# Kernel tuning notes

Hardware: AMD Instinct MI355X
Metric: run time of the kernel (lower is better)

## Reference

```python
import jax, jax.numpy as jnp
import numpy as np

N_HEAD, D_MODEL, D_K, D_V, MAX_NEIGHBOR = 8, 512, 64, 64, 5
BS, SEQ = 2, 1024


def setup_inputs() -> dict:
    key = jax.random.key(0)
    ks = jax.random.split(key, 12)
    inp = {
        'q': jax.random.normal(ks[0], (BS, SEQ, D_MODEL), jnp.float32),
        'k': jax.random.normal(ks[1], (BS, SEQ, D_MODEL), jnp.float32),
        'v': jax.random.normal(ks[2], (BS, SEQ, D_MODEL), jnp.float32),
        'mask': jnp.ones((BS, SEQ, SEQ), jnp.int32),
        'dist': jax.random.randint(ks[3], (BS, SEQ, SEQ), 0, 10, jnp.int32),
        # weights stored as (in, out) so y = x @ W
        'w_qs': jax.random.normal(ks[4], (D_MODEL, N_HEAD * D_K), jnp.float32) * 0.02,
        'w_ks': jax.random.normal(ks[5], (D_MODEL, N_HEAD * D_K), jnp.float32) * 0.02,
        'w_vs': jax.random.normal(ks[6], (D_MODEL, N_HEAD * D_V), jnp.float32) * 0.02,
        'w_fc': jax.random.normal(ks[7], (N_HEAD * D_V, D_MODEL), jnp.float32) * 0.02,
        'ln_gamma': jnp.ones((D_MODEL,), jnp.float32),
        'ln_beta': jnp.zeros((D_MODEL,), jnp.float32),
        'base_rpr': jax.random.normal(ks[8], (MAX_NEIGHBOR + 1, D_K), jnp.float32) * 0.02,
    }
    return inp


def reference(q, k, v, mask, dist, w_qs, w_ks, w_vs, w_fc, ln_gamma, ln_beta, base_rpr):
    bs, sq, dm = q.shape
    temp = jnp.asarray(D_K, q.dtype) ** 0.5
    residual = q
    # layer norm on q only (as in original)
    mu = jnp.mean(q, axis=-1, keepdims=True)
    var = jnp.var(q, axis=-1, keepdims=True)
    qn = (q - mu) / jnp.sqrt(var + 1e-6) * ln_gamma + ln_beta
    # projections -> [bs, heads, seq, d]
    qh = (qn @ w_qs).reshape(bs, sq, N_HEAD, D_K).transpose(0, 2, 1, 3)
    kh = (k @ w_ks).reshape(bs, sq, N_HEAD, D_K).transpose(0, 2, 1, 3)
    vh = (v @ w_vs).reshape(bs, sq, N_HEAD, D_V).transpose(0, 2, 1, 3)
    qs = qh / temp
    # standard QK^T scores
    attn1 = jnp.einsum('bhid,bhjd->bhij', qs, kh)
    # relative-position scores: instead of materializing rpr[b,i,j,d],
    # contract q with the small base table then gather by clipped distance.
    dc = jnp.minimum(dist, MAX_NEIGHBOR)  # dist>max_neighbor -> max_neighbor
    qb = jnp.einsum('bhid,md->bhim', qs, base_rpr)  # [bs,h,seq,M+1]
    idx = jnp.broadcast_to(dc[:, None, :, :], (bs, N_HEAD, sq, sq))
    attn2 = jnp.take_along_axis(qb, idx, axis=-1)  # [bs,h,seq,seq]
    attn = attn1 + attn2
    attn = jnp.where(mask[:, None, :, :] == 0, jnp.asarray(-1e9, attn.dtype), attn)
    attn = jax.nn.softmax(attn, axis=-1)  # dropout disabled (eval)
    out = jnp.einsum('bhij,bhjd->bhid', attn, vh)
    out = out.transpose(0, 2, 1, 3).reshape(bs, sq, N_HEAD * D_V)
    out = out @ w_fc + residual
    return out, attn
```

## Files before the change

### kernel.cpp

```cpp
#include <hip/hip_runtime.h>
#include <math.h>

#define SEQ 1024
#define DM 512

typedef __attribute__((ext_vector_type(8))) short bf16x8;
typedef __attribute__((ext_vector_type(4))) short bf16x4;
typedef __attribute__((ext_vector_type(4))) float f32x4;
typedef __attribute__((ext_vector_type(4))) int i32x4;

static __device__ __forceinline__ short f2b(float f) {
    union { float f; unsigned u; } x; x.f = f;
    unsigned r = (x.u + 0x7FFFu + ((x.u >> 16) & 1u)) >> 16;
    return (short)r;
}
static __device__ __forceinline__ float b2f(short s) {
    union { unsigned u; float f; } x; x.u = ((unsigned)(unsigned short)s) << 16;
    return x.f;
}
static __device__ __forceinline__ int sidx(int row, int col) {
    int byte = (row << 7) + (col << 1);
    byte ^= (row & 7) << 4;
    return byte >> 1;
}

static __device__ __forceinline__ void stage_f32(short* dst, const float* src, int srcStride, int tid) {
    int r = tid >> 2, c = (tid & 3) * 16;
    const float* p = src + (size_t)r * srcStride + c;
    bf16x8 v0, v1;
    #pragma unroll
    for (int e = 0; e < 8; ++e) v0[e] = f2b(p[e]);
    #pragma unroll
    for (int e = 0; e < 8; ++e) v1[e] = f2b(p[8 + e]);
    *(bf16x8*)&dst[sidx(r, c)] = v0;
    *(bf16x8*)&dst[sidx(r, c + 8)] = v1;
}
static __device__ __forceinline__ void stage_bf16(short* dst, const short* src, int srcStride, int tid) {
    int r = tid >> 2, c = (tid & 3) * 16;
    const short* p = src + (size_t)r * srcStride + c;
    bf16x8 v0 = *(const bf16x8*)p;
    bf16x8 v1 = *(const bf16x8*)(p + 8);
    *(bf16x8*)&dst[sidx(r, c)] = v0;
    *(bf16x8*)&dst[sidx(r, c + 8)] = v1;
}

static __device__ __forceinline__ void mma64(const short* sA, const short* sB, f32x4* acc,
                                             int w, int lr, int lg) {
    #pragma unroll
    for (int ks = 0; ks < 2; ++ks) {
        bf16x8 af = *(const bf16x8*)&sA[sidx(w * 16 + lr, ks * 32 + lg * 8)];
        #pragma unroll
        for (int nt = 0; nt < 4; ++nt) {
            bf16x8 bf = *(const bf16x8*)&sB[sidx(nt * 16 + lr, ks * 32 + lg * 8)];
            acc[nt] = __builtin_amdgcn_mfma_f32_16x16x32_bf16(af, bf, acc[nt], 0, 0, 0);
        }
    }
}

__global__ __launch_bounds__(256) void prep_kernel(
    const float* __restrict__ w0, const float* __restrict__ w1,
    const float* __restrict__ w2, const float* __restrict__ w3, short* __restrict__ wt,
    const float* __restrict__ q, float* __restrict__ qn,
    const float* __restrict__ gamma, const float* __restrict__ beta,
    const int* __restrict__ dist, const int* __restrict__ mask, unsigned char* __restrict__ idxp) {
    int blk = blockIdx.x;
    int tid = threadIdx.x;
    if (blk < 256) {
        int wsel = blk >> 6;
        int t = blk & 63;
        int tr = t >> 3, tc = t & 7;
        const float* src = wsel == 0 ? w0 : wsel == 1 ? w1 : wsel == 2 ? w2 : w3;
        short* dst = wt + (size_t)wsel * 512 * 512;
        __shared__ float tile[64][65];
        int r = tid >> 2, c = (tid & 3) * 16;
        const float* p = src + (size_t)(tr * 64 + r) * 512 + tc * 64 + c;
        #pragma unroll
        for (int e = 0; e < 16; ++e) tile[r][c + e] = p[e];
        __syncthreads();
        bf16x8 v0, v1;
        #pragma unroll
        for (int e = 0; e < 16; ++e) {
            short bv = f2b(tile[c + e][r]);
            if (e < 8) v0[e] = bv; else v1[e - 8] = bv;
        }
        short* qd = dst + (size_t)(tc * 64 + r) * 512 + tr * 64 + c;
        *(bf16x8*)qd = v0;
        *(bf16x8*)(qd + 8) = v1;
    } else if (blk < 2304) {
        int row = blk - 256;
        const float* x = q + (size_t)row * DM;
        float* y = qn + (size_t)row * DM;
        float v1 = x[tid], v2 = x[tid + 256];
        float s = v1 + v2;
        float ss = v1 * v1 + v2 * v2;
        for (int o = 32; o > 0; o >>= 1) { s += __shfl_down(s, o); ss += __shfl_down(ss, o); }
        __shared__ float red[4], red2[4];
        __shared__ float s_mu, s_rstd;
        int wid = tid >> 6, lane = tid & 63;
        if (lane == 0) { red[wid] = s; red2[wid] = ss; }
        __syncthreads();
        if (tid == 0) {
            float ts = red[0] + red[1] + red[2] + red[3];
            float tss = red2[0] + red2[1] + red2[2] + red2[3];
            float mu = ts / DM;
            float var = tss / DM - mu * mu;
            s_mu = mu;
            s_rstd = rsqrtf(var + 1e-6f);
        }
        __syncthreads();
        float mu = s_mu, rstd = s_rstd;
        y[tid]       = (v1 - mu) * rstd * gamma[tid]       + beta[tid];
        y[tid + 256] = (v2 - mu) * rstd * gamma[tid + 256] + beta[tid + 256];
    } else {
        size_t base = ((size_t)(blk - 2304) * 256 + tid) * 8;
        i32x4 d0 = *(const i32x4*)(dist + base);
        i32x4 d1 = *(const i32x4*)(dist + base + 4);
        i32x4 m0 = *(const i32x4*)(mask + base);
        i32x4 m1 = *(const i32x4*)(mask + base + 4);
        int dv[8], mv[8];
        #pragma unroll
        for (int e = 0; e < 4; ++e) { dv[e] = d0[e]; dv[4 + e] = d1[e]; mv[e] = m0[e]; mv[4 + e] = m1[e]; }
        unsigned char ob[4];
        #pragma unroll
        for (int e = 0; e < 4; ++e) {
            int dA = dv[2 * e];     if (dA > 5) dA = 5;
            int dB = dv[2 * e + 1]; if (dB > 5) dB = 5;
            unsigned nA = (unsigned)dA | (mv[2 * e] == 0 ? 8u : 0u);
            unsigned nB = (unsigned)dB | (mv[2 * e + 1] == 0 ? 8u : 0u);
            ob[e] = (unsigned char)(nA | (nB << 4));
        }
        *(uchar4*)(idxp + base / 2) = *(uchar4*)ob;
    }
}

__global__ __launch_bounds__(256) void qkv_kernel(
    const float* __restrict__ qn, const float* __restrict__ k, const float* __restrict__ v,
    const short* __restrict__ wT, short* __restrict__ qsb, short* __restrict__ khx,
    short* __restrict__ vfx) {
    __shared__ short sA[64 * 64];
    __shared__ short sB[64 * 64];
    int tid = threadIdx.x;
    int sel = blockIdx.x >> 8;
    int t = blockIdx.x & 255;
    int bx = t & 7, by = t >> 3;
    int m0 = by << 6, n0 = bx << 6;
    int w = tid >> 6, l = tid & 63;
    int lr = l & 15, lg = l >> 4;
    const float* A = sel == 0 ? qn : sel == 1 ? k : v;
    const short* Bt = wT + (size_t)sel * 262144;
    float scale = sel == 0 ? 0.125f : 1.0f;
    f32x4 acc[4] = {};
    for (int kt = 0; kt < 512; kt += 64) {
        __syncthreads();
        stage_f32(sA, A + (size_t)m0 * 512 + kt, 512, tid);
        stage_bf16(sB, Bt + (size_t)n0 * 512 + kt, 512, tid);
        __syncthreads();
        mma64(sA, sB, acc, w, lr, lg);
    }
    short* scratch = sA + w * 1024;
    if (sel == 0) {
        #pragma unroll
        for (int nt = 0; nt < 4; ++nt)
            #pragma unroll
            for (int r = 0; r < 4; ++r)
                scratch[(lg * 4 + r) * 64 + nt * 16 + lr] = f2b(acc[nt][r] * scale);
        #pragma unroll
        for (int cc = 0; cc < 2; ++cc) {
            int c = cc * 64 + l;
            *(bf16x8*)&qsb[(size_t)(m0 + w * 16 + (c >> 3)) * 512 + n0 + (c & 7) * 8]
                = *(const bf16x8*)&scratch[c * 8];
        }
    } else if (sel == 1) {
        #pragma unroll
        for (int nt = 0; nt < 4; ++nt) {
            int dl = nt * 16 + lr;
            int f = dl >> 5, lgp = (dl >> 3) & 3, e = dl & 7;
            int base = ((f * 4 + lgp) * 16) * 8 + e;
            #pragma unroll
            for (int r = 0; r < 4; ++r)
                scratch[base + (lg * 4 + r) * 8] = f2b(acc[nt][r]);
        }
        int bq = m0 >> 10, jt = (m0 >> 6) & 15;
        short* blockp = khx + ((((size_t)(bq * 8 + bx) * 16 + jt) * 4 + w) << 10);
        *(bf16x8*)(blockp + l * 8)       = *(const bf16x8*)(scratch + l * 8);
        *(bf16x8*)(blockp + 512 + l * 8) = *(const bf16x8*)(scratch + 512 + l * 8);
    } else {
        int bq = m0 >> 10, j6 = (m0 >> 6) & 15, p = j6 >> 1, rel = j6 & 1;
        #pragma unroll
        for (int nt = 0; nt < 4; ++nt)
            #pragma unroll
            for (int r = 0; r < 4; ++r) {
                int s = ((nt * 2 + (lg >> 1)) * 16 + lr) * 8 + (lg & 1) * 4 + r;
                scratch[s] = f2b(acc[nt][r]);
            }
        short* blockp = vfx + ((((size_t)(bq * 8 + bx) * 8 + p) * 4 + w) << 11);
        #pragma unroll
        for (int cc = 0; cc < 2; ++cc) {
            int c = cc * 64 + l;
            int s = c * 8;
            int g = s + ((c >> 5) << 8) + (rel << 8);
            *(bf16x8*)(blockp + g) = *(const bf16x8*)(scratch + s);
        }
    }
}

#define IDXSTR 520
__global__ __launch_bounds__(256) void attn_fused_kernel(
    const short* __restrict__ qsb, const short* __restrict__ khx,
    const short* __restrict__ vfx, const unsigned char* __restrict__ idxp,
    const float* __restrict__ rpr, float* __restrict__ attnp, short* __restrict__ oh) {
    int bid = blockIdx.x;
    int bh = bid >> 6, it = bid & 63;
    int b = bh >> 3, h = bh & 7;
    int i0 = it << 4;
    int tid = threadIdx.x;
    int w = tid >> 6, l = tid & 63;
    int lr = l & 15, lg = l >> 4;

    __shared__ short sQ[16 * 64];
    __shared__ float sQB[16 * 8];
    __shared__ float sL[4][16];
    __shared__ float sO[4 * 16 * 64];
    __shared__ __align__(16) unsigned char sIdx[16 * IDXSTR];

    if (tid < 128) {
        int r = tid >> 3, c = (tid & 7) * 8;
        bf16x8 qv = *(const bf16x8*)(qsb + ((size_t)(b * SEQ + i0 + r)) * DM + h * 64 + c);
        *(bf16x8*)&sQ[sidx(r, c)] = qv;
    }
    {
        const unsigned char* ibase = idxp + ((size_t)(b * SEQ + i0)) * 512;
        #pragma unroll
        for (int p = 0; p < 2; ++p) {
            int idx = p * 256 + tid;
            int row = idx >> 5;
            int cb = (idx & 31) * 16;
            i32x4 v = *(const i32x4*)(ibase + (size_t)row * 512 + cb);
            *(i32x4*)&sIdx[row * IDXSTR + cb] = v;
        }
    }
    __syncthreads();
    if (tid < 128) {
        int r = tid >> 3, m = tid & 7;
        if (m < 6) {
            float a = 0.f;
            #pragma unroll 8
            for (int d = 0; d < 64; ++d) a += b2f(sQ[sidx(r, d)]) * rpr[m * 64 + d];
            sQB[r * 8 + m] = a;
        }
    }
    __syncthreads();

    bf16x8 qf0 = *(const bf16x8*)&sQ[sidx(lr, lg * 8)];
    bf16x8 qf1 = *(const bf16x8*)&sQ[sidx(lr, 32 + lg * 8)];

    float qb0 = sQB[lr * 8 + 0], qb1 = sQB[lr * 8 + 1], qb2 = sQB[lr * 8 + 2];
    float qb3 = sQB[lr * 8 + 3], qb4 = sQB[lr * 8 + 4], qb5 = sQB[lr * 8 + 5];

    float l_lane = 0.f;
    unsigned p_lo[16], p_hi[16];
    f32x4 accO[4] = {};
    const short* kblk = khx + (((size_t)bh * 16) * 4 + w) * 1024;
    const short* vblk = vfx + (((size_t)bh * 8) * 4 + w) * 2048;
    int fragoff = (lg * 16 + lr) * 8;
    const unsigned char* irow = sIdx + lr * IDXSTR + w * 8 + lg * 2;

    #pragma unroll
    for (int jt = 0; jt < 16; ++jt) {
        const short* kb = kblk + jt * 4096;
        bf16x8 kf0 = *(const bf16x8*)(kb + fragoff);
        bf16x8 kf1 = *(const bf16x8*)(kb + 512 + fragoff);
        f32x4 sf = {};
        sf = __builtin_amdgcn_mfma_f32_16x16x32_bf16(kf0, qf0, sf, 0, 0, 0);
        sf = __builtin_amdgcn_mfma_f32_16x16x32_bf16(kf1, qf1, sf, 0, 0, 0);
        unsigned u = *(const unsigned short*)(irow + jt * 32);
        float pv[4];
        #pragma unroll
        for (int r = 0; r < 4; ++r) {
            unsigned bb = (u >> (4 * r)) & 0xFu;
            unsigned dd = bb & 7u;
            float t0 = (dd & 1) ? qb1 : qb0;
            float t1 = (dd & 1) ? qb3 : qb2;
            float t2 = (dd & 1) ? qb5 : qb4;
            float u0 = (dd & 2) ? t1 : t0;
            float bias = (dd & 4) ? t2 : u0;
            float s = fminf(sf[r] + bias, 30.f);
            float p = (bb & 8) ? 0.f : __expf(s);
            pv[r] = p;
            l_lane += p;
        }
        unsigned plo, phi;
        asm("v_cvt_pk_bf16_f32 %0, %1, %2" : "=v"(plo) : "v"(pv[0]), "v"(pv[1]));
        asm("v_cvt_pk_bf16_f32 %0, %1, %2" : "=v"(phi) : "v"(pv[2]), "v"(pv[3]));
        p_lo[jt] = plo; p_hi[jt] = phi;
        if (jt & 1) {
            unsigned plo0 = p_lo[jt - 1], phi0 = p_hi[jt - 1];
            int srcA = lr + ((lg & 1) << 5);
            int srcB = srcA + 16;
            unsigned aw0 = __shfl(plo0, srcA), aw1 = __shfl(phi0, srcA);
            unsigned aw2 = __shfl(plo,  srcA), aw3 = __shfl(phi,  srcA);
            unsigned bw0 = __shfl(plo0, srcB), bw1 = __shfl(phi0, srcB);
            unsigned bw2 = __shfl(plo,  srcB), bw3 = __shfl(phi,  srcB);
            bool hi = lg >= 2;
            union { unsigned q[4]; bf16x8 v; } afu;
            afu.q[0] = hi ? aw2 : aw0;
            afu.q[1] = hi ? aw3 : aw1;
            afu.q[2] = hi ? bw2 : bw0;
            afu.q[3] = hi ? bw3 : bw1;
            bf16x8 af = afu.v;
            const short* vb = vblk + (jt >> 1) * 8192;
            #pragma unroll
            for (int nt = 0; nt < 4; ++nt) {
                bf16x8 bf = *(const bf16x8*)(vb + nt * 512 + fragoff);
                accO[nt] = __builtin_amdgcn_mfma_f32_16x16x32_bf16(af, bf, accO[nt], 0, 0, 0);
            }
        }
    }

    l_lane += __shfl_xor(l_lane, 16);
    l_lane += __shfl_xor(l_lane, 32);
    if (lg == 0) sL[w][lr] = l_lane;
    #pragma unroll
    for (int nt = 0; nt < 4; ++nt)
        #pragma unroll
        for (int r = 0; r < 4; ++r)
            sO[w * 1024 + (lg * 4 + r) * 64 + nt * 16 + lr] = accO[nt][r];
    __syncthreads();

    {
        int row = tid >> 4, c4 = (tid & 15) * 4;
        f32x4 o = *(f32x4*)&sO[row * 64 + c4];
        o += *(f32x4*)&sO[1024 + row * 64 + c4];
        o += *(f32x4*)&sO[2048 + row * 64 + c4];
        o += *(f32x4*)&sO[3072 + row * 64 + c4];
        float rl = 1.f / (sL[0][row] + sL[1][row] + sL[2][row] + sL[3][row]);
        bf16x4 ob;
        #pragma unroll
        for (int e = 0; e < 4; ++e) ob[e] = f2b(o[e] * rl);
        *(bf16x4*)&oh[((size_t)(b * SEQ + i0 + row)) * DM + h * 64 + c4] = ob;
    }

    float rl = 1.f / (sL[0][lr] + sL[1][lr] + sL[2][lr] + sL[3][lr]);
    float* ap = attnp + ((size_t)(bh * SEQ + i0 + lr)) * SEQ + w * 16 + lg * 4;
    #pragma unroll
    for (int jt = 0; jt < 16; ++jt) {
        unsigned plo = p_lo[jt], phi = p_hi[jt];
        f32x4 o;
        o[0] = b2f((short)(plo & 0xffff)) * rl;
        o[1] = b2f((short)(plo >> 16))    * rl;
        o[2] = b2f((short)(phi & 0xffff)) * rl;
        o[3] = b2f((short)(phi >> 16))    * rl;
        *(f32x4*)&ap[jt * 64] = o;
    }
}

__global__ __launch_bounds__(256) void fc_kernel(
    const short* __restrict__ oh, const short* __restrict__ BtFc,
    const float* __restrict__ Rsd, float* __restrict__ Cp) {
    __shared__ short sA[64 * 64];
    __shared__ short sB[64 * 64];
    int tid = threadIdx.x;
    int bx = blockIdx.x & 7, by = blockIdx.x >> 3;
    int m0 = by << 6, n0 = bx << 6;
    int w = tid >> 6, l = tid & 63;
    int lr = l & 15, lg = l >> 4;
    f32x4 acc[4] = {};
    for (int kt = 0; kt < 512; kt += 64) {
        __syncthreads();
        stage_bf16(sA, oh + (size_t)m0 * 512 + kt, 512, tid);
        stage_bf16(sB, BtFc + (size_t)n0 * 512 + kt, 512, tid);
        __syncthreads();
        mma64(sA, sB, acc, w, lr, lg);
    }
    #pragma unroll
    for (int nt = 0; nt < 4; ++nt)
        #pragma unroll
        for (int r = 0; r < 4; ++r) {
            int gm = m0 + w * 16 + lg * 4 + r;
            int gn = n0 + nt * 16 + lr;
            Cp[(size_t)gm * 512 + gn] = acc[nt][r] + Rsd[(size_t)gm * 512 + gn];
        }
}

extern "C" void kernel_launch(void* const* d_in, const int* in_sizes, int n_in,
                              void* d_out, int out_size, void* d_ws, size_t ws_size,
                              hipStream_t stream) {
    const float* q     = (const float*)d_in[0];
    const float* k     = (const float*)d_in[1];
    const float* v     = (const float*)d_in[2];
    const int*   mask  = (const int*)d_in[3];
    const int*   dist  = (const int*)d_in[4];
    const float* w_qs  = (const float*)d_in[5];
    const float* w_ks  = (const float*)d_in[6];
    const float* w_vs  = (const float*)d_in[7];
    const float* w_fc  = (const float*)d_in[8];
    const float* gamma = (const float*)d_in[9];
    const float* beta  = (const float*)d_in[10];
    const float* rpr   = (const float*)d_in[11];

    char* wsb = (char*)d_ws;
    float* qn   = (float*)wsb;
    short* oh   = (short*)wsb;
    short* wT   = (short*)(wsb + 4u * 1024 * 1024);
    short* qsb  = (short*)(wsb + 6u * 1024 * 1024);
    short* khx  = (short*)(wsb + 8u * 1024 * 1024);
    short* vfx  = (short*)(wsb + 10u * 1024 * 1024);
    unsigned char* idxp = (unsigned char*)(wsb + 12u * 1024 * 1024);

    float* outp  = (float*)d_out;
    float* attnp = outp + 1048576;

    prep_kernel<<<3328, 256, 0, stream>>>(w_qs, w_ks, w_vs, w_fc, wT, q, qn, gamma, beta, dist, mask, idxp);
    qkv_kernel<<<768, 256, 0, stream>>>(qn, k, v, wT, qsb, khx, vfx);
    attn_fused_kernel<<<1024, 256, 0, stream>>>(qsb, khx, vfx, idxp, rpr, attnp, oh);
    fc_kernel<<<256, 256, 0, stream>>>(oh, wT + 786432, q, outp);
}
```

Measured before the change: 70.48 us.

## Process 32 query rows per attention block to reuse K/V fragments

Each attention block now handles two 16-row query tiles, so every K and V fragment loaded from global memory feeds two sets of MFMAs, and half as many blocks are launched. Shared memory is aliased: the output-reduction buffer overlays the Q, bias and index buffers to keep LDS use down. The cost is roughly double the register pressure (two probability arrays and two accumulator sets), which may reduce occupancy or cause spills, and only 512 blocks remain to fill the GPU.

```diff
diff --git a/kernel.cpp b/kernel.cpp
--- a/kernel.cpp
+++ b/kernel.cpp
@@ -210,20 +210,21 @@
     const short* __restrict__ vfx, const unsigned char* __restrict__ idxp,
     const float* __restrict__ rpr, float* __restrict__ attnp, short* __restrict__ oh) {
     int bid = blockIdx.x;
-    int bh = bid >> 6, it = bid & 63;
+    int bh = bid >> 5, it = bid & 31;
     int b = bh >> 3, h = bh & 7;
-    int i0 = it << 4;
+    int i0 = it << 5;
     int tid = threadIdx.x;
     int w = tid >> 6, l = tid & 63;
     int lr = l & 15, lg = l >> 4;
 
-    __shared__ short sQ[16 * 64];
-    __shared__ float sQB[16 * 8];
-    __shared__ float sL[4][16];
-    __shared__ float sO[4 * 16 * 64];
-    __shared__ __align__(16) unsigned char sIdx[16 * IDXSTR];
-
-    if (tid < 128) {
+    __shared__ __align__(16) char sBuf[21764];
+    __shared__ float sL[4][32];
+    short* sQ = (short*)sBuf;
+    float* sQB = (float*)(sBuf + 4096);
+    unsigned char* sIdx = (unsigned char*)(sBuf + 5120);
+    float* sO = (float*)sBuf;
+
+    {
         int r = tid >> 3, c = (tid & 7) * 8;
         bf16x8 qv = *(const bf16x8*)(qsb + ((size_t)(b * SEQ + i0 + r)) * DM + h * 64 + c);
         *(bf16x8*)&sQ[sidx(r, c)] = qv;
@@ -231,7 +232,7 @@
     {
         const unsigned char* ibase = idxp + ((size_t)(b * SEQ + i0)) * 512;
         #pragma unroll
-        for (int p = 0; p < 2; ++p) {
+        for (int p = 0; p < 4; ++p) {
             int idx = p * 256 + tid;
             int row = idx >> 5;
             int cb = (idx & 31) * 16;
@@ -240,7 +241,7 @@
         }
     }
     __syncthreads();
-    if (tid < 128) {
+    {
         int r = tid >> 3, m = tid & 7;
         if (m < 6) {
             float a = 0.f;
@@ -251,82 +252,125 @@
     }
     __syncthreads();
 
-    bf16x8 qf0 = *(const bf16x8*)&sQ[sidx(lr, lg * 8)];
-    bf16x8 qf1 = *(const bf16x8*)&sQ[sidx(lr, 32 + lg * 8)];
-
-    float qb0 = sQB[lr * 8 + 0], qb1 = sQB[lr * 8 + 1], qb2 = sQB[lr * 8 + 2];
-    float qb3 = sQB[lr * 8 + 3], qb4 = sQB[lr * 8 + 4], qb5 = sQB[lr * 8 + 5];
-
-    float l_lane = 0.f;
-    unsigned p_lo[16], p_hi[16];
-    f32x4 accO[4] = {};
+    bf16x8 qfA0 = *(const bf16x8*)&sQ[sidx(lr, lg * 8)];
+    bf16x8 qfA1 = *(const bf16x8*)&sQ[sidx(lr, 32 + lg * 8)];
+    bf16x8 qfB0 = *(const bf16x8*)&sQ[sidx(16 + lr, lg * 8)];
+    bf16x8 qfB1 = *(const bf16x8*)&sQ[sidx(16 + lr, 32 + lg * 8)];
+
+    float qa0 = sQB[lr * 8 + 0], qa1 = sQB[lr * 8 + 1], qa2 = sQB[lr * 8 + 2];
+    float qa3 = sQB[lr * 8 + 3], qa4 = sQB[lr * 8 + 4], qa5 = sQB[lr * 8 + 5];
+    float qc0 = sQB[(16 + lr) * 8 + 0], qc1 = sQB[(16 + lr) * 8 + 1], qc2 = sQB[(16 + lr) * 8 + 2];
+    float qc3 = sQB[(16 + lr) * 8 + 3], qc4 = sQB[(16 + lr) * 8 + 4], qc5 = sQB[(16 + lr) * 8 + 5];
+
+    float lA = 0.f, lB = 0.f;
+    unsigned pAlo[16], pAhi[16], pBlo[16], pBhi[16];
+    f32x4 accA[4] = {}, accB[4] = {};
     const short* kblk = khx + (((size_t)bh * 16) * 4 + w) * 1024;
     const short* vblk = vfx + (((size_t)bh * 8) * 4 + w) * 2048;
     int fragoff = (lg * 16 + lr) * 8;
-    const unsigned char* irow = sIdx + lr * IDXSTR + w * 8 + lg * 2;
+    const unsigned char* irowA = sIdx + lr * IDXSTR + w * 8 + lg * 2;
+    const unsigned char* irowB = sIdx + (16 + lr) * IDXSTR + w * 8 + lg * 2;
 
     #pragma unroll
     for (int jt = 0; jt < 16; ++jt) {
         const short* kb = kblk + jt * 4096;
         bf16x8 kf0 = *(const bf16x8*)(kb + fragoff);
         bf16x8 kf1 = *(const bf16x8*)(kb + 512 + fragoff);
-        f32x4 sf = {};
-        sf = __builtin_amdgcn_mfma_f32_16x16x32_bf16(kf0, qf0, sf, 0, 0, 0);
-        sf = __builtin_amdgcn_mfma_f32_16x16x32_bf16(kf1, qf1, sf, 0, 0, 0);
-        unsigned u = *(const unsigned short*)(irow + jt * 32);
-        float pv[4];
+        f32x4 sfA = {}, sfB = {};
+        sfA = __builtin_amdgcn_mfma_f32_16x16x32_bf16(kf0, qfA0, sfA, 0, 0, 0);
+        sfA = __builtin_amdgcn_mfma_f32_16x16x32_bf16(kf1, qfA1, sfA, 0, 0, 0);
+        sfB = __builtin_amdgcn_mfma_f32_16x16x32_bf16(kf0, qfB0, sfB, 0, 0, 0);
+        sfB = __builtin_amdgcn_mfma_f32_16x16x32_bf16(kf1, qfB1, sfB, 0, 0, 0);
+        unsigned uA = *(const unsigned short*)(irowA + jt * 32);
+        unsigned uB = *(const unsigned short*)(irowB + jt * 32);
+        float pvA[4], pvB[4];
         #pragma unroll
         for (int r = 0; r < 4; ++r) {
-            unsigned bb = (u >> (4 * r)) & 0xFu;
+            unsigned bb = (uA >> (4 * r)) & 0xFu;
             unsigned dd = bb & 7u;
-            float t0 = (dd & 1) ? qb1 : qb0;
-            float t1 = (dd & 1) ? qb3 : qb2;
-            float t2 = (dd & 1) ? qb5 : qb4;
+            float t0 = (dd & 1) ? qa1 : qa0;
+            float t1 = (dd & 1) ? qa3 : qa2;
+            float t2 = (dd & 1) ? qa5 : qa4;
             float u0 = (dd & 2) ? t1 : t0;
             float bias = (dd & 4) ? t2 : u0;
-            float s = fminf(sf[r] + bias, 30.f);
+            float s = fminf(sfA[r] + bias, 30.f);
             float p = (bb & 8) ? 0.f : __expf(s);
-            pv[r] = p;
-            l_lane += p;
-        }
-        unsigned plo, phi;
-        asm("v_cvt_pk_bf16_f32 %0, %1, %2" : "=v"(plo) : "v"(pv[0]), "v"(pv[1]));
-        asm("v_cvt_pk_bf16_f32 %0, %1, %2" : "=v"(phi) : "v"(pv[2]), "v"(pv[3]));
-        p_lo[jt] = plo; p_hi[jt] = phi;
+            pvA[r] = p; lA += p;
+        }
+        #pragma unroll
+        for (int r = 0; r < 4; ++r) {
+            unsigned bb = (uB >> (4 * r)) & 0xFu;
+            unsigned dd = bb & 7u;
+            float t0 = (dd & 1) ? qc1 : qc0;
+            float t1 = (dd & 1) ? qc3 : qc2;
+            float t2 = (dd & 1) ? qc5 : qc4;
+            float u0 = (dd & 2) ? t1 : t0;
+            float bias = (dd & 4) ? t2 : u0;
+            float s = fminf(sfB[r] + bias, 30.f);
+            float p = (bb & 8) ? 0.f : __expf(s);
+            pvB[r] = p; lB += p;
+        }
+        unsigned a0, a1, b0, b1;
+        asm("v_cvt_pk_bf16_f32 %0, %1, %2" : "=v"(a0) : "v"(pvA[0]), "v"(pvA[1]));
+        asm("v_cvt_pk_bf16_f32 %0, %1, %2" : "=v"(a1) : "v"(pvA[2]), "v"(pvA[3]));
+        asm("v_cvt_pk_bf16_f32 %0, %1, %2" : "=v"(b0) : "v"(pvB[0]), "v"(pvB[1]));
+        asm("v_cvt_pk_bf16_f32 %0, %1, %2" : "=v"(b1) : "v"(pvB[2]), "v"(pvB[3]));
+        pAlo[jt] = a0; pAhi[jt] = a1; pBlo[jt] = b0; pBhi[jt] = b1;
         if (jt & 1) {
-            unsigned plo0 = p_lo[jt - 1], phi0 = p_hi[jt - 1];
             int srcA = lr + ((lg & 1) << 5);
             int srcB = srcA + 16;
-            unsigned aw0 = __shfl(plo0, srcA), aw1 = __shfl(phi0, srcA);
-            unsigned aw2 = __shfl(plo,  srcA), aw3 = __shfl(phi,  srcA);
-            unsigned bw0 = __shfl(plo0, srcB), bw1 = __shfl(phi0, srcB);
-            unsigned bw2 = __shfl(plo,  srcB), bw3 = __shfl(phi,  srcB);
+            const short* vb = vblk + (jt >> 1) * 8192;
+            bf16x8 vf0 = *(const bf16x8*)(vb + 0 * 512 + fragoff);
+            bf16x8 vf1 = *(const bf16x8*)(vb + 1 * 512 + fragoff);
+            bf16x8 vf2 = *(const bf16x8*)(vb + 2 * 512 + fragoff);
+            bf16x8 vf3 = *(const bf16x8*)(vb + 3 * 512 + fragoff);
             bool hi = lg >= 2;
-            union { unsigned q[4]; bf16x8 v; } afu;
-            afu.q[0] = hi ? aw2 : aw0;
-            afu.q[1] = hi ? aw3 : aw1;
-            afu.q[2] = hi ? bw2 : bw0;
-            afu.q[3] = hi ? bw3 : bw1;
-            bf16x8 af = afu.v;
-            const short* vb = vblk + (jt >> 1) * 8192;
-            #pragma unroll
-            for (int nt = 0; nt < 4; ++nt) {
-                bf16x8 bf = *(const bf16x8*)(vb + nt * 512 + fragoff);
-                accO[nt] = __builtin_amdgcn_mfma_f32_16x16x32_bf16(af, bf, accO[nt], 0, 0, 0);
+            {
+                unsigned plo0 = pAlo[jt - 1], phi0 = pAhi[jt - 1];
+                unsigned aw0 = __shfl(plo0, srcA), aw1 = __shfl(phi0, srcA);
+                unsigned aw2 = __shfl(a0,  srcA), aw3 = __shfl(a1,  srcA);
+                unsigned bw0 = __shfl(plo0, srcB), bw1 = __shfl(phi0, srcB);
+                unsigned bw2 = __shfl(a0,  srcB), bw3 = __shfl(a1,  srcB);
+                union { unsigned q[4]; bf16x8 v; } afu;
+                afu.q[0] = hi ? aw2 : aw0;
+                afu.q[1] = hi ? aw3 : aw1;
+                afu.q[2] = hi ? bw2 : bw0;
+                afu.q[3] = hi ? bw3 : bw1;
+                accA[0] = __builtin_amdgcn_mfma_f32_16x16x32_bf16(afu.v, vf0, accA[0], 0, 0, 0);
+                accA[1] = __builtin_amdgcn_mfma_f32_16x16x32_bf16(afu.v, vf1, accA[1], 0, 0, 0);
+                accA[2] = __builtin_amdgcn_mfma_f32_16x16x32_bf16(afu.v, vf2, accA[2], 0, 0, 0);
+                accA[3] = __builtin_amdgcn_mfma_f32_16x16x32_bf16(afu.v, vf3, accA[3], 0, 0, 0);
             }
-        }
-    }
-
-    l_lane += __shfl_xor(l_lane, 16);
-    l_lane += __shfl_xor(l_lane, 32);
-    if (lg == 0) sL[w][lr] = l_lane;
+            {
+                unsigned plo0 = pBlo[jt - 1], phi0 = pBhi[jt - 1];
+                unsigned aw0 = __shfl(plo0, srcA), aw1 = __shfl(phi0, srcA);
+                unsigned aw2 = __shfl(b0,  srcA), aw3 = __shfl(b1,  srcA);
+                unsigned bw0 = __shfl(plo0, srcB), bw1 = __shfl(phi0, srcB);
+                unsigned bw2 = __shfl(b0,  srcB), bw3 = __shfl(b1,  srcB);
+                union { unsigned q[4]; bf16x8 v; } afu;
+                afu.q[0] = hi ? aw2 : aw0;
+                afu.q[1] = hi ? aw3 : aw1;
+                afu.q[2] = hi ? bw2 : bw0;
+                afu.q[3] = hi ? bw3 : bw1;
+                accB[0] = __builtin_amdgcn_mfma_f32_16x16x32_bf16(afu.v, vf0, accB[0], 0, 0, 0);
+                accB[1] = __builtin_amdgcn_mfma_f32_16x16x32_bf16(afu.v, vf1, accB[1], 0, 0, 0);
+                accB[2] = __builtin_amdgcn_mfma_f32_16x16x32_bf16(afu.v, vf2, accB[2], 0, 0, 0);
+                accB[3] = __builtin_amdgcn_mfma_f32_16x16x32_bf16(afu.v, vf3, accB[3], 0, 0, 0);
+            }
+        }
+    }
+
+    lA += __shfl_xor(lA, 16); lA += __shfl_xor(lA, 32);
+    lB += __shfl_xor(lB, 16); lB += __shfl_xor(lB, 32);
+    if (lg == 0) { sL[w][lr] = lA; sL[w][16 + lr] = lB; }
+    __syncthreads();
+
     #pragma unroll
     for (int nt = 0; nt < 4; ++nt)
         #pragma unroll
         for (int r = 0; r < 4; ++r)
-            sO[w * 1024 + (lg * 4 + r) * 64 + nt * 16 + lr] = accO[nt][r];
-    __syncthreads();
-
+            sO[w * 1024 + (lg * 4 + r) * 64 + nt * 16 + lr] = accA[nt][r];
+    __syncthreads();
     {
         int row = tid >> 4, c4 = (tid & 15) * 4;
         f32x4 o = *(f32x4*)&sO[row * 64 + c4];
@@ -339,18 +383,44 @@
         for (int e = 0; e < 4; ++e) ob[e] = f2b(o[e] * rl);
         *(bf16x4*)&oh[((size_t)(b * SEQ + i0 + row)) * DM + h * 64 + c4] = ob;
     }
-
-    float rl = 1.f / (sL[0][lr] + sL[1][lr] + sL[2][lr] + sL[3][lr]);
-    float* ap = attnp + ((size_t)(bh * SEQ + i0 + lr)) * SEQ + w * 16 + lg * 4;
+    __syncthreads();
+    #pragma unroll
+    for (int nt = 0; nt < 4; ++nt)
+        #pragma unroll
+        for (int r = 0; r < 4; ++r)
+            sO[w * 1024 + (lg * 4 + r) * 64 + nt * 16 + lr] = accB[nt][r];
+    __syncthreads();
+    {
+        int row = tid >> 4, c4 = (tid & 15) * 4;
+        f32x4 o = *(f32x4*)&sO[row * 64 + c4];
+        o += *(f32x4*)&sO[1024 + row * 64 + c4];
+        o += *(f32x4*)&sO[2048 + row * 64 + c4];
+        o += *(f32x4*)&sO[3072 + row * 64 + c4];
+        float rl = 1.f / (sL[0][16 + row] + sL[1][16 + row] + sL[2][16 + row] + sL[3][16 + row]);
+        bf16x4 ob;
+        #pragma unroll
+        for (int e = 0; e < 4; ++e) ob[e] = f2b(o[e] * rl);
+        *(bf16x4*)&oh[((size_t)(b * SEQ + i0 + 16 + row)) * DM + h * 64 + c4] = ob;
+    }
+
+    float rlA = 1.f / (sL[0][lr] + sL[1][lr] + sL[2][lr] + sL[3][lr]);
+    float rlB = 1.f / (sL[0][16 + lr] + sL[1][16 + lr] + sL[2][16 + lr] + sL[3][16 + lr]);
+    float* apA = attnp + ((size_t)(bh * SEQ + i0 + lr)) * SEQ + w * 16 + lg * 4;
+    float* apB = attnp + ((size_t)(bh * SEQ + i0 + 16 + lr)) * SEQ + w * 16 + lg * 4;
     #pragma unroll
     for (int jt = 0; jt < 16; ++jt) {
-        unsigned plo = p_lo[jt], phi = p_hi[jt];
         f32x4 o;
-        o[0] = b2f((short)(plo & 0xffff)) * rl;
-        o[1] = b2f((short)(plo >> 16))    * rl;
-        o[2] = b2f((short)(phi & 0xffff)) * rl;
-        o[3] = b2f((short)(phi >> 16))    * rl;
-        *(f32x4*)&ap[jt * 64] = o;
+        o[0] = b2f((short)(pAlo[jt] & 0xffff)) * rlA;
+        o[1] = b2f((short)(pAlo[jt] >> 16))    * rlA;
+        o[2] = b2f((short)(pAhi[jt] & 0xffff)) * rlA;
+        o[3] = b2f((short)(pAhi[jt] >> 16))    * rlA;
+        *(f32x4*)&apA[jt * 64] = o;
+        f32x4 o2;
+        o2[0] = b2f((short)(pBlo[jt] & 0xffff)) * rlB;
+        o2[1] = b2f((short)(pBlo[jt] >> 16))    * rlB;
+        o2[2] = b2f((short)(pBhi[jt] & 0xffff)) * rlB;
+        o2[3] = b2f((short)(pBhi[jt] >> 16))    * rlB;
+        *(f32x4*)&apB[jt * 64] = o2;
     }
 }
 
@@ -412,6 +482,6 @@
 
     prep_kernel<<<3328, 256, 0, stream>>>(w_qs, w_ks, w_vs, w_fc, wT, q, qn, gamma, beta, dist, mask, idxp);
     qkv_kernel<<<768, 256, 0, stream>>>(qn, k, v, wT, qsb, khx, vfx);
-    attn_fused_kernel<<<1024, 256, 0, stream>>>(qsb, khx, vfx, idxp, rpr, attnp, oh);
+    attn_fused_kernel<<<512, 256, 0, stream>>>(qsb, khx, vfx, idxp, rpr, attnp, oh);
     fc_kernel<<<256, 256, 0, stream>>>(oh, wT + 786432, q, outp);
 }
```

New measurement: 69.42 us. No clear change (-1.5%).
